# Optimization experiments

Measured on AMD Instinct MI355X. Metric: run time of the kernel, lower is better.

The kernel has to match this reference:

```python
import jax, jax.numpy as jnp
import numpy as np
from jax import lax

BATCH = 8192
DIM = 2048
NUM_STATES = 3


def setup_inputs() -> dict:
    key = jax.random.key(0)
    k1, k2, k3, k4 = jax.random.split(key, 4)
    y = jax.random.randint(k1, (BATCH, DIM), 0, 2, dtype=jnp.int64 if jax.config.jax_enable_x64 else jnp.int32)
    transition_probs = jax.random.normal(k2, (NUM_STATES, NUM_STATES), dtype=jnp.float32)
    emission_probs = jax.random.normal(k3, (NUM_STATES, 2), dtype=jnp.float32)
    start_probs = jax.random.normal(k4, (NUM_STATES,), dtype=jnp.float32)
    return {
        "y": y,
        "transition_probs": transition_probs,
        "emission_probs": emission_probs,
        "start_probs": start_probs,
    }


def reference(y, transition_probs, emission_probs, start_probs):
    # Normalize parameters in log space (matches torch.log_softmax)
    log_T = jax.nn.log_softmax(transition_probs, axis=-1)   # [S, S]
    log_E = jax.nn.log_softmax(emission_probs, axis=-1)     # [S, 2]
    log_pi = jax.nn.log_softmax(start_probs, axis=-1)       # [S]

    # Gather per-timestep emission log-probs: [B, DIM, S]
    em = log_E.T[y]

    # alpha_0[b, s] = log_pi[s] + log_E[s, y[b,0]]
    alpha0 = log_pi[None, :] + em[:, 0]                      # [B, S]

    def step(alpha, em_t):
        # alpha[b, i] + log_T[i, j] -> logsumexp over i, plus emission at t
        new = jax.nn.logsumexp(alpha[:, :, None] + log_T[None, :, :], axis=1) + em_t
        return new, None

    # Scan over time: em[:, 1:] moved to leading time axis -> [DIM-1, B, S]
    alpha_T, _ = lax.scan(step, alpha0, jnp.moveaxis(em[:, 1:], 1, 0))

    log_prob = jax.nn.logsumexp(alpha_T, axis=-1)            # [B]
    return log_prob.mean()
```

## Files before the change

### kernel.cpp

```cpp
#include <hip/hip_runtime.h>
#include <math.h>

#define BATCH 8192
#define DIM   2048

__global__ __launch_bounds__(256, 6)
void hmm_fwd(const int* __restrict__ y,
             const float* __restrict__ tp,
             const float* __restrict__ ep,
             const float* __restrict__ sp,
             float* __restrict__ row_lp)
{
    __shared__ __align__(16) float t4[16 * 12];
    __shared__ __align__(16) float t8[256 * 12];
    __shared__ __align__(16) unsigned char ystage[4][512];
    __shared__ float vlds[3];

    const int tid  = threadIdx.x;
    const int lane = tid & 63;
    const int wid  = tid >> 6;
    const int b    = blockIdx.x * 4 + wid;

    {
        const int* __restrict__ p = y + (size_t)b * DIM + lane * 4;
        unsigned char* __restrict__ row = ystage[wid];
        #pragma unroll
        for (int g = 0; g < 8; ++g) {
            int4 v = *reinterpret_cast<const int4*>(p + g * 256);
            row[64*g + lane] =
                (unsigned char)(v.x | (v.y<<1) | (v.z<<2) | (v.w<<3));
        }
    }

    if (wid == 0) {
        float T[3][3], E[3][2], pi[3];
        #pragma unroll
        for (int i = 0; i < 3; ++i) {
            float a0 = tp[i*3+0], a1 = tp[i*3+1], a2 = tp[i*3+2];
            float mx = fmaxf(a0, fmaxf(a1, a2));
            float e0 = __expf(a0-mx), e1 = __expf(a1-mx), e2 = __expf(a2-mx);
            float inv = 1.0f / (e0+e1+e2);
            T[i][0] = e0*inv; T[i][1] = e1*inv; T[i][2] = e2*inv;
        }
        #pragma unroll
        for (int s = 0; s < 3; ++s) {
            float a0 = ep[s*2+0], a1 = ep[s*2+1];
            float mx = fmaxf(a0, a1);
            float e0 = __expf(a0-mx), e1 = __expf(a1-mx);
            float inv = 1.0f / (e0+e1);
            E[s][0] = e0*inv; E[s][1] = e1*inv;
        }
        {
            float a0 = sp[0], a1 = sp[1], a2 = sp[2];
            float mx = fmaxf(a0, fmaxf(a1, a2));
            float e0 = __expf(a0-mx), e1 = __expf(a1-mx), e2 = __expf(a2-mx);
            float inv = 1.0f / (e0+e1+e2);
            pi[0] = e0*inv; pi[1] = e1*inv; pi[2] = e2*inv;
        }

        if (lane == 0) {
            float c00 =  (T[1][1]*T[2][2] - T[1][2]*T[2][1]);
            float c01 = -(T[1][0]*T[2][2] - T[1][2]*T[2][0]);
            float c02 =  (T[1][0]*T[2][1] - T[1][1]*T[2][0]);
            float c10 = -(T[0][1]*T[2][2] - T[0][2]*T[2][1]);
            float c11 =  (T[0][0]*T[2][2] - T[0][2]*T[2][0]);
            float c12 = -(T[0][0]*T[2][1] - T[0][1]*T[2][0]);
            float c20 =  (T[0][1]*T[1][2] - T[0][2]*T[1][1]);
            float c21 = -(T[0][0]*T[1][2] - T[0][2]*T[1][0]);
            float c22 =  (T[0][0]*T[1][1] - T[0][1]*T[1][0]);
            float det = T[0][0]*c00 + T[0][1]*c01 + T[0][2]*c02;
            float invd = 1.0f / det;
            vlds[0] = (pi[0]*c00 + pi[1]*c01 + pi[2]*c02) * invd;
            vlds[1] = (pi[0]*c10 + pi[1]*c11 + pi[2]*c12) * invd;
            vlds[2] = (pi[0]*c20 + pi[1]*c21 + pi[2]*c22) * invd;
        }

        float M0[9], M1[9];
        #pragma unroll
        for (int k = 0; k < 3; ++k)
            #pragma unroll
            for (int j = 0; j < 3; ++j) {
                M0[k*3+j] = T[k][j] * E[j][0];
                M1[k*3+j] = T[k][j] * E[j][1];
            }

        if (lane < 16) {
            int code = lane;
            float A[9];
            const float* F0 = (code & 1) ? M1 : M0;
            #pragma unroll
            for (int e = 0; e < 9; ++e) A[e] = F0[e];
            code >>= 1;
            #pragma unroll
            for (int s = 1; s < 4; ++s) {
                const float* F = (code & 1) ? M1 : M0;
                code >>= 1;
                float Z[9];
                #pragma unroll
                for (int i = 0; i < 3; ++i)
                    #pragma unroll
                    for (int j = 0; j < 3; ++j)
                        Z[i*3+j] = fmaf(A[i*3+0], F[0*3+j],
                                   fmaf(A[i*3+1], F[1*3+j], A[i*3+2]*F[2*3+j]));
                #pragma unroll
                for (int e = 0; e < 9; ++e) A[e] = Z[e];
            }
            #pragma unroll
            for (int e = 0; e < 9; ++e) t4[lane*12 + e] = A[e];
        }
    }
    __syncthreads();

    {
        const float4* A4 = reinterpret_cast<const float4*>(&t4[(tid & 15) * 12]);
        const float4* B4 = reinterpret_cast<const float4*>(&t4[(tid >> 4) * 12]);
        float4 a0 = A4[0], a1 = A4[1], a2 = A4[2];
        float4 b0 = B4[0], b1 = B4[1], b2 = B4[2];
        float A[9] = {a0.x,a0.y,a0.z, a0.w,a1.x,a1.y, a1.z,a1.w,a2.x};
        float B[9] = {b0.x,b0.y,b0.z, b0.w,b1.x,b1.y, b1.z,b1.w,b2.x};
        float Z[9];
        #pragma unroll
        for (int i = 0; i < 3; ++i)
            #pragma unroll
            for (int j = 0; j < 3; ++j)
                Z[i*3+j] = fmaf(A[i*3+0], B[0*3+j],
                           fmaf(A[i*3+1], B[1*3+j], A[i*3+2]*B[2*3+j]));
        #pragma unroll
        for (int e = 0; e < 9; ++e) t8[tid*12 + e] = Z[e];
    }
    __syncthreads();

    uint2 q = *reinterpret_cast<const uint2*>(&ystage[wid][8 * lane]);

    float R[9] = {1.f,0.f,0.f, 0.f,1.f,0.f, 0.f,0.f,1.f};
    float lsc = 0.0f;

    #pragma unroll
    for (int j = 0; j < 4; ++j) {
        unsigned w  = (j < 2) ? q.x : q.y;
        unsigned sh = (j & 1) * 16;
        int idx = (int)(((w >> sh) & 15u) | ((w >> (sh + 4)) & 0xF0u));
        const float4* G4 = reinterpret_cast<const float4*>(&t8[idx * 12]);
        float4 p0 = G4[0], p1 = G4[1], p2 = G4[2];
        float g0 = p0.x, g1 = p0.y, g2 = p0.z,
              g3 = p0.w, g4 = p1.x, g5 = p1.y,
              g6 = p1.z, g7 = p1.w, g8 = p2.x;
        float nR[9];
        #pragma unroll
        for (int i = 0; i < 3; ++i) {
            nR[i*3+0] = fmaf(R[i*3+0], g0, fmaf(R[i*3+1], g3, R[i*3+2]*g6));
            nR[i*3+1] = fmaf(R[i*3+0], g1, fmaf(R[i*3+1], g4, R[i*3+2]*g7));
            nR[i*3+2] = fmaf(R[i*3+0], g2, fmaf(R[i*3+1], g5, R[i*3+2]*g8));
        }
        #pragma unroll
        for (int e = 0; e < 9; ++e) R[e] = nR[e];

        if (j == 1 || j == 3) {
            float m = R[0];
            #pragma unroll
            for (int e = 1; e < 9; ++e) m = fmaxf(m, R[e]);
            lsc += __logf(m);
            float inv = 1.0f / m;
            #pragma unroll
            for (int e = 0; e < 9; ++e) R[e] *= inv;
        }
    }

    #pragma unroll
    for (int o = 1; o < 64; o <<= 1) {
        float S[9];
        #pragma unroll
        for (int e = 0; e < 9; ++e) S[e] = __shfl_down(R[e], o, 64);
        float osc = __shfl_down(lsc, o, 64);
        float nR[9];
        #pragma unroll
        for (int i = 0; i < 3; ++i)
            #pragma unroll
            for (int j = 0; j < 3; ++j)
                nR[i*3+j] = fmaf(R[i*3+0], S[0*3+j],
                            fmaf(R[i*3+1], S[1*3+j], R[i*3+2]*S[2*3+j]));
        #pragma unroll
        for (int e = 0; e < 9; ++e) R[e] = nR[e];
        lsc += osc;
    }

    if (lane == 0) {
        float r0 = R[0] + R[1] + R[2];
        float r1 = R[3] + R[4] + R[5];
        float r2 = R[6] + R[7] + R[8];
        float p  = fmaf(vlds[0], r0, fmaf(vlds[1], r1, vlds[2] * r2));
        row_lp[b] = __logf(p) + lsc;
    }
}

__global__ void reduce_mean(const float* __restrict__ row, float* __restrict__ out)
{
    float s = 0.0f;
    for (int i = threadIdx.x; i < BATCH; i += 1024) s += row[i];
    #pragma unroll
    for (int o = 32; o > 0; o >>= 1) s += __shfl_down(s, o, 64);
    __shared__ float sm[16];
    int w = threadIdx.x >> 6;
    if ((threadIdx.x & 63) == 0) sm[w] = s;
    __syncthreads();
    if (threadIdx.x == 0) {
        float t = 0.0f;
        #pragma unroll
        for (int i = 0; i < 16; ++i) t += sm[i];
        out[0] = t * (1.0f / BATCH);
    }
}

extern "C" void kernel_launch(void* const* d_in, const int* in_sizes, int n_in,
                              void* d_out, int out_size, void* d_ws, size_t ws_size,
                              hipStream_t stream)
{
    const int*   y  = (const int*)d_in[0];
    const float* tp = (const float*)d_in[1];
    const float* ep = (const float*)d_in[2];
    const float* sp = (const float*)d_in[3];
    float* out = (float*)d_out;
    float* row = (float*)d_ws;

    hmm_fwd<<<BATCH/4, 256, 0, stream>>>(y, tp, ep, sp, row);
    reduce_mean<<<1, 1024, 0, stream>>>(row, out);
}
```

Before: 101.9 us.

## Hoist transition-table build into prep kernel and use DPP/swizzle reduction shuffles

The 256-entry table of 8-step products (and the stationary-vector weights) was rebuilt in every block. It is now computed once by a separate single-block kernel into workspace, and each block just copies it from global/L2 into shared memory. The table stride changes from 12 to 13 floats, which avoids LDS bank conflicts on the data-dependent gathers but gives up float4 loads. The warp-level matrix-product reduction switches from `__shfl_down` to xor-butterfly DPP, ds_swizzle and permlane32 swaps. The cost is one extra kernel launch and a 13 KB global copy per block.

```diff
diff --git a/kernel.cpp b/kernel.cpp
--- a/kernel.cpp
+++ b/kernel.cpp
@@ -4,17 +4,181 @@
 #define BATCH 8192
 #define DIM   2048
 
+#define TSTR 13
+#define TBL_FLOATS (256 * TSTR + 4)
+
+__device__ __forceinline__ float sh_x1(float x) {
+#if __has_builtin(__builtin_amdgcn_update_dpp)
+    return __uint_as_float((unsigned)__builtin_amdgcn_update_dpp(
+        0, (int)__float_as_uint(x), 0xB1, 0xF, 0xF, false));
+#else
+    return __shfl_xor(x, 1, 64);
+#endif
+}
+__device__ __forceinline__ float sh_x2(float x) {
+#if __has_builtin(__builtin_amdgcn_update_dpp)
+    return __uint_as_float((unsigned)__builtin_amdgcn_update_dpp(
+        0, (int)__float_as_uint(x), 0x4E, 0xF, 0xF, false));
+#else
+    return __shfl_xor(x, 2, 64);
+#endif
+}
+__device__ __forceinline__ float sh_x4(float x) {
+#if __has_builtin(__builtin_amdgcn_ds_swizzle)
+    return __uint_as_float((unsigned)__builtin_amdgcn_ds_swizzle(
+        (int)__float_as_uint(x), 0x101F));
+#else
+    return __shfl_xor(x, 4, 64);
+#endif
+}
+__device__ __forceinline__ float sh_x8(float x) {
+#if __has_builtin(__builtin_amdgcn_ds_swizzle)
+    return __uint_as_float((unsigned)__builtin_amdgcn_ds_swizzle(
+        (int)__float_as_uint(x), 0x201F));
+#else
+    return __shfl_xor(x, 8, 64);
+#endif
+}
+__device__ __forceinline__ float sh_x16(float x) {
+#if __has_builtin(__builtin_amdgcn_ds_swizzle)
+    return __uint_as_float((unsigned)__builtin_amdgcn_ds_swizzle(
+        (int)__float_as_uint(x), 0x401F));
+#else
+    return __shfl_xor(x, 16, 64);
+#endif
+}
+__device__ __forceinline__ float sh_d32(float x) {
+#if __has_builtin(__builtin_amdgcn_permlane32_swap)
+    auto r = __builtin_amdgcn_permlane32_swap(
+        __float_as_uint(x), __float_as_uint(x), false, false);
+    return __uint_as_float(r[1]);
+#else
+    return __shfl_down(x, 32, 64);
+#endif
+}
+
+#define RSTAGE(SHUF) do {                                                   \
+    float S[9];                                                             \
+    _Pragma("unroll")                                                       \
+    for (int e = 0; e < 9; ++e) S[e] = SHUF(R[e]);                          \
+    float osc = SHUF(lsc);                                                  \
+    float nR[9];                                                            \
+    _Pragma("unroll")                                                       \
+    for (int i = 0; i < 3; ++i) {                                           \
+        nR[i*3+0] = fmaf(R[i*3+0], S[0], fmaf(R[i*3+1], S[3], R[i*3+2]*S[6])); \
+        nR[i*3+1] = fmaf(R[i*3+0], S[1], fmaf(R[i*3+1], S[4], R[i*3+2]*S[7])); \
+        nR[i*3+2] = fmaf(R[i*3+0], S[2], fmaf(R[i*3+1], S[5], R[i*3+2]*S[8])); \
+    }                                                                       \
+    _Pragma("unroll")                                                       \
+    for (int e = 0; e < 9; ++e) R[e] = nR[e];                               \
+    lsc += osc;                                                             \
+} while (0)
+
+__global__ void hmm_prep(const float* __restrict__ tp,
+                         const float* __restrict__ ep,
+                         const float* __restrict__ sp,
+                         float* __restrict__ tbl)
+{
+    __shared__ float t4s[16 * TSTR];
+    const int tid = threadIdx.x;
+
+    float T[3][3], E[3][2], pi[3];
+    #pragma unroll
+    for (int i = 0; i < 3; ++i) {
+        float a0 = tp[i*3+0], a1 = tp[i*3+1], a2 = tp[i*3+2];
+        float mx = fmaxf(a0, fmaxf(a1, a2));
+        float e0 = __expf(a0-mx), e1 = __expf(a1-mx), e2 = __expf(a2-mx);
+        float inv = 1.0f / (e0+e1+e2);
+        T[i][0] = e0*inv; T[i][1] = e1*inv; T[i][2] = e2*inv;
+    }
+    #pragma unroll
+    for (int s = 0; s < 3; ++s) {
+        float a0 = ep[s*2+0], a1 = ep[s*2+1];
+        float mx = fmaxf(a0, a1);
+        float e0 = __expf(a0-mx), e1 = __expf(a1-mx);
+        float inv = 1.0f / (e0+e1);
+        E[s][0] = e0*inv; E[s][1] = e1*inv;
+    }
+    {
+        float a0 = sp[0], a1 = sp[1], a2 = sp[2];
+        float mx = fmaxf(a0, fmaxf(a1, a2));
+        float e0 = __expf(a0-mx), e1 = __expf(a1-mx), e2 = __expf(a2-mx);
+        float inv = 1.0f / (e0+e1+e2);
+        pi[0] = e0*inv; pi[1] = e1*inv; pi[2] = e2*inv;
+    }
+
+    if (tid == 0) {
+        float c00 =  (T[1][1]*T[2][2] - T[1][2]*T[2][1]);
+        float c01 = -(T[1][0]*T[2][2] - T[1][2]*T[2][0]);
+        float c02 =  (T[1][0]*T[2][1] - T[1][1]*T[2][0]);
+        float c10 = -(T[0][1]*T[2][2] - T[0][2]*T[2][1]);
+        float c11 =  (T[0][0]*T[2][2] - T[0][2]*T[2][0]);
+        float c12 = -(T[0][0]*T[2][1] - T[0][1]*T[2][0]);
+        float c20 =  (T[0][1]*T[1][2] - T[0][2]*T[1][1]);
+        float c21 = -(T[0][0]*T[1][2] - T[0][2]*T[1][0]);
+        float c22 =  (T[0][0]*T[1][1] - T[0][1]*T[1][0]);
+        float det = T[0][0]*c00 + T[0][1]*c01 + T[0][2]*c02;
+        float invd = 1.0f / det;
+        tbl[256*TSTR + 0] = (pi[0]*c00 + pi[1]*c01 + pi[2]*c02) * invd;
+        tbl[256*TSTR + 1] = (pi[0]*c10 + pi[1]*c11 + pi[2]*c12) * invd;
+        tbl[256*TSTR + 2] = (pi[0]*c20 + pi[1]*c21 + pi[2]*c22) * invd;
+        tbl[256*TSTR + 3] = 0.0f;
+    }
+
+    if (tid < 16) {
+        float M0[9], M1[9];
+        #pragma unroll
+        for (int k = 0; k < 3; ++k)
+            #pragma unroll
+            for (int j = 0; j < 3; ++j) {
+                M0[k*3+j] = T[k][j] * E[j][0];
+                M1[k*3+j] = T[k][j] * E[j][1];
+            }
+        int code = tid;
+        float A[9];
+        const float* F0 = (code & 1) ? M1 : M0;
+        #pragma unroll
+        for (int e = 0; e < 9; ++e) A[e] = F0[e];
+        code >>= 1;
+        #pragma unroll
+        for (int s = 1; s < 4; ++s) {
+            const float* F = (code & 1) ? M1 : M0;
+            code >>= 1;
+            float Z[9];
+            #pragma unroll
+            for (int i = 0; i < 3; ++i)
+                #pragma unroll
+                for (int j = 0; j < 3; ++j)
+                    Z[i*3+j] = fmaf(A[i*3+0], F[0*3+j],
+                               fmaf(A[i*3+1], F[1*3+j], A[i*3+2]*F[2*3+j]));
+            #pragma unroll
+            for (int e = 0; e < 9; ++e) A[e] = Z[e];
+        }
+        #pragma unroll
+        for (int e = 0; e < 9; ++e) t4s[tid*TSTR + e] = A[e];
+    }
+    __syncthreads();
+
+    const float* A  = &t4s[(tid & 15) * TSTR];
+    const float* Bm = &t4s[(tid >> 4) * TSTR];
+    float Z[9];
+    #pragma unroll
+    for (int i = 0; i < 3; ++i)
+        #pragma unroll
+        for (int j = 0; j < 3; ++j)
+            Z[i*3+j] = fmaf(A[i*3+0], Bm[0*3+j],
+                       fmaf(A[i*3+1], Bm[1*3+j], A[i*3+2]*Bm[2*3+j]));
+    #pragma unroll
+    for (int e = 0; e < 9; ++e) tbl[tid*TSTR + e] = Z[e];
+}
+
 __global__ __launch_bounds__(256, 6)
 void hmm_fwd(const int* __restrict__ y,
-             const float* __restrict__ tp,
-             const float* __restrict__ ep,
-             const float* __restrict__ sp,
+             const float* __restrict__ tbl,
              float* __restrict__ row_lp)
 {
-    __shared__ __align__(16) float t4[16 * 12];
-    __shared__ __align__(16) float t8[256 * 12];
+    __shared__ __align__(16) float t8s[TBL_FLOATS];
     __shared__ __align__(16) unsigned char ystage[4][512];
-    __shared__ float vlds[3];
 
     const int tid  = threadIdx.x;
     const int lane = tid & 63;
@@ -32,101 +196,14 @@
         }
     }
 
-    if (wid == 0) {
-        float T[3][3], E[3][2], pi[3];
-        #pragma unroll
-        for (int i = 0; i < 3; ++i) {
-            float a0 = tp[i*3+0], a1 = tp[i*3+1], a2 = tp[i*3+2];
-            float mx = fmaxf(a0, fmaxf(a1, a2));
-            float e0 = __expf(a0-mx), e1 = __expf(a1-mx), e2 = __expf(a2-mx);
-            float inv = 1.0f / (e0+e1+e2);
-            T[i][0] = e0*inv; T[i][1] = e1*inv; T[i][2] = e2*inv;
-        }
-        #pragma unroll
-        for (int s = 0; s < 3; ++s) {
-            float a0 = ep[s*2+0], a1 = ep[s*2+1];
-            float mx = fmaxf(a0, a1);
-            float e0 = __expf(a0-mx), e1 = __expf(a1-mx);
-            float inv = 1.0f / (e0+e1);
-            E[s][0] = e0*inv; E[s][1] = e1*inv;
-        }
-        {
-            float a0 = sp[0], a1 = sp[1], a2 = sp[2];
-            float mx = fmaxf(a0, fmaxf(a1, a2));
-            float e0 = __expf(a0-mx), e1 = __expf(a1-mx), e2 = __expf(a2-mx);
-            float inv = 1.0f / (e0+e1+e2);
-            pi[0] = e0*inv; pi[1] = e1*inv; pi[2] = e2*inv;
-        }
-
-        if (lane == 0) {
-            float c00 =  (T[1][1]*T[2][2] - T[1][2]*T[2][1]);
-            float c01 = -(T[1][0]*T[2][2] - T[1][2]*T[2][0]);
-            float c02 =  (T[1][0]*T[2][1] - T[1][1]*T[2][0]);
-            float c10 = -(T[0][1]*T[2][2] - T[0][2]*T[2][1]);
-            float c11 =  (T[0][0]*T[2][2] - T[0][2]*T[2][0]);
-            float c12 = -(T[0][0]*T[2][1] - T[0][1]*T[2][0]);
-            float c20 =  (T[0][1]*T[1][2] - T[0][2]*T[1][1]);
-            float c21 = -(T[0][0]*T[1][2] - T[0][2]*T[1][0]);
-            float c22 =  (T[0][0]*T[1][1] - T[0][1]*T[1][0]);
-            float det = T[0][0]*c00 + T[0][1]*c01 + T[0][2]*c02;
-            float invd = 1.0f / det;
-            vlds[0] = (pi[0]*c00 + pi[1]*c01 + pi[2]*c02) * invd;
-            vlds[1] = (pi[0]*c10 + pi[1]*c11 + pi[2]*c12) * invd;
-            vlds[2] = (pi[0]*c20 + pi[1]*c21 + pi[2]*c22) * invd;
-        }
-
-        float M0[9], M1[9];
-        #pragma unroll
-        for (int k = 0; k < 3; ++k)
-            #pragma unroll
-            for (int j = 0; j < 3; ++j) {
-                M0[k*3+j] = T[k][j] * E[j][0];
-                M1[k*3+j] = T[k][j] * E[j][1];
-            }
-
-        if (lane < 16) {
-            int code = lane;
-            float A[9];
-            const float* F0 = (code & 1) ? M1 : M0;
-            #pragma unroll
-            for (int e = 0; e < 9; ++e) A[e] = F0[e];
-            code >>= 1;
-            #pragma unroll
-            for (int s = 1; s < 4; ++s) {
-                const float* F = (code & 1) ? M1 : M0;
-                code >>= 1;
-                float Z[9];
-                #pragma unroll
-                for (int i = 0; i < 3; ++i)
-                    #pragma unroll
-                    for (int j = 0; j < 3; ++j)
-                        Z[i*3+j] = fmaf(A[i*3+0], F[0*3+j],
-                                   fmaf(A[i*3+1], F[1*3+j], A[i*3+2]*F[2*3+j]));
-                #pragma unroll
-                for (int e = 0; e < 9; ++e) A[e] = Z[e];
-            }
-            #pragma unroll
-            for (int e = 0; e < 9; ++e) t4[lane*12 + e] = A[e];
-        }
-    }
-    __syncthreads();
-
     {
-        const float4* A4 = reinterpret_cast<const float4*>(&t4[(tid & 15) * 12]);
-        const float4* B4 = reinterpret_cast<const float4*>(&t4[(tid >> 4) * 12]);
-        float4 a0 = A4[0], a1 = A4[1], a2 = A4[2];
-        float4 b0 = B4[0], b1 = B4[1], b2 = B4[2];
-        float A[9] = {a0.x,a0.y,a0.z, a0.w,a1.x,a1.y, a1.z,a1.w,a2.x};
-        float B[9] = {b0.x,b0.y,b0.z, b0.w,b1.x,b1.y, b1.z,b1.w,b2.x};
-        float Z[9];
-        #pragma unroll
-        for (int i = 0; i < 3; ++i)
-            #pragma unroll
-            for (int j = 0; j < 3; ++j)
-                Z[i*3+j] = fmaf(A[i*3+0], B[0*3+j],
-                           fmaf(A[i*3+1], B[1*3+j], A[i*3+2]*B[2*3+j]));
-        #pragma unroll
-        for (int e = 0; e < 9; ++e) t8[tid*12 + e] = Z[e];
+        const float4* __restrict__ src = reinterpret_cast<const float4*>(tbl);
+        float4* __restrict__ dst = reinterpret_cast<float4*>(t8s);
+        #pragma unroll
+        for (int g = 0; g < 4; ++g) {
+            int i = tid + g * 256;
+            if (i < TBL_FLOATS / 4) dst[i] = src[i];
+        }
     }
     __syncthreads();
 
@@ -140,11 +217,10 @@
         unsigned w  = (j < 2) ? q.x : q.y;
         unsigned sh = (j & 1) * 16;
         int idx = (int)(((w >> sh) & 15u) | ((w >> (sh + 4)) & 0xF0u));
-        const float4* G4 = reinterpret_cast<const float4*>(&t8[idx * 12]);
-        float4 p0 = G4[0], p1 = G4[1], p2 = G4[2];
-        float g0 = p0.x, g1 = p0.y, g2 = p0.z,
-              g3 = p0.w, g4 = p1.x, g5 = p1.y,
-              g6 = p1.z, g7 = p1.w, g8 = p2.x;
+        const float* gp = &t8s[idx * TSTR];
+        float g0 = gp[0], g1 = gp[1], g2 = gp[2],
+              g3 = gp[3], g4 = gp[4], g5 = gp[5],
+              g6 = gp[6], g7 = gp[7], g8 = gp[8];
         float nR[9];
         #pragma unroll
         for (int i = 0; i < 3; ++i) {
@@ -166,29 +242,19 @@
         }
     }
 
-    #pragma unroll
-    for (int o = 1; o < 64; o <<= 1) {
-        float S[9];
-        #pragma unroll
-        for (int e = 0; e < 9; ++e) S[e] = __shfl_down(R[e], o, 64);
-        float osc = __shfl_down(lsc, o, 64);
-        float nR[9];
-        #pragma unroll
-        for (int i = 0; i < 3; ++i)
-            #pragma unroll
-            for (int j = 0; j < 3; ++j)
-                nR[i*3+j] = fmaf(R[i*3+0], S[0*3+j],
-                            fmaf(R[i*3+1], S[1*3+j], R[i*3+2]*S[2*3+j]));
-        #pragma unroll
-        for (int e = 0; e < 9; ++e) R[e] = nR[e];
-        lsc += osc;
-    }
+    RSTAGE(sh_x1);
+    RSTAGE(sh_x2);
+    RSTAGE(sh_x4);
+    RSTAGE(sh_x8);
+    RSTAGE(sh_x16);
+    RSTAGE(sh_d32);
 
     if (lane == 0) {
         float r0 = R[0] + R[1] + R[2];
         float r1 = R[3] + R[4] + R[5];
         float r2 = R[6] + R[7] + R[8];
-        float p  = fmaf(vlds[0], r0, fmaf(vlds[1], r1, vlds[2] * r2));
+        const float* v = &t8s[256 * TSTR];
+        float p = fmaf(v[0], r0, fmaf(v[1], r1, v[2] * r2));
         row_lp[b] = __logf(p) + lsc;
     }
 }
@@ -221,7 +287,9 @@
     const float* sp = (const float*)d_in[3];
     float* out = (float*)d_out;
     float* row = (float*)d_ws;
-
-    hmm_fwd<<<BATCH/4, 256, 0, stream>>>(y, tp, ep, sp, row);
+    float* tbl = (float*)d_ws + BATCH;
+
+    hmm_prep<<<1, 256, 0, stream>>>(tp, ep, sp, tbl);
+    hmm_fwd<<<BATCH/4, 256, 0, stream>>>(y, tbl, row);
     reduce_mean<<<1, 1024, 0, stream>>>(row, out);
 }
```

Result: slower. 105.5 us (+3.5%).
